# Optimization experiments

Hardware: AMD Instinct MI355X
Metric: run time of the kernel (lower is better)

Reference implementation:

```python
import jax, jax.numpy as jnp
import numpy as np

N_NODES = 100000
N_EDGES = 1600000
D_IN = 128
D_HID = 128
D_OUT = 128


def setup_inputs() -> dict:
    key = jax.random.key(0)
    ks = jax.random.split(key, 9)
    x = jax.random.normal(ks[0], (N_NODES, D_IN), dtype=jnp.float32)
    src = jax.random.randint(ks[1], (N_EDGES,), 0, N_NODES, dtype=jnp.int32)
    dst = jax.random.randint(ks[2], (N_EDGES,), 0, N_NODES, dtype=jnp.int32)
    s = 1.0 / np.sqrt(D_IN)
    Wc = jax.random.uniform(ks[3], (D_IN, D_HID), dtype=jnp.float32, minval=-s, maxval=s)
    bc = jnp.zeros((D_HID,), dtype=jnp.float32)
    s1 = 1.0 / np.sqrt(D_HID)
    W1 = jax.random.uniform(ks[4], (D_HID, D_HID), dtype=jnp.float32, minval=-s1, maxval=s1)
    b1 = jax.random.uniform(ks[5], (D_HID,), dtype=jnp.float32, minval=-s1, maxval=s1)
    W2 = jax.random.uniform(ks[6], (D_HID, D_OUT), dtype=jnp.float32, minval=-s1, maxval=s1)
    b2 = jax.random.uniform(ks[7], (D_OUT,), dtype=jnp.float32, minval=-s1, maxval=s1)
    return {"x": x, "src": src, "dst": dst, "Wc": Wc, "bc": bc,
            "W1": W1, "b1": b1, "W2": W2, "b2": b2}


def reference(x, src, dst, Wc, bc, W1, b1, W2, b2):
    # DGL GraphConv with norm='both' (default), no edge_weight:
    #   h = x / sqrt(out_deg(src));  agg[v] = sum_{(u->v)} h[u];  agg /= sqrt(in_deg(v))
    ones = jnp.ones((src.shape[0],), dtype=x.dtype)
    deg_out = jax.ops.segment_sum(ones, src, num_segments=N_NODES)
    deg_in = jax.ops.segment_sum(ones, dst, num_segments=N_NODES)
    norm_out = jax.lax.rsqrt(jnp.clip(deg_out, 1.0))[:, None]  # [N,1]
    norm_in = jax.lax.rsqrt(jnp.clip(deg_in, 1.0))[:, None]

    h = x * norm_out
    msgs = h[src]                                              # [E, D_in]
    agg = jax.ops.segment_sum(msgs, dst, num_segments=N_NODES) # [N, D_in]
    agg = agg * norm_in
    h = agg @ Wc + bc                                          # GraphConv linear

    # num_layers == 2 path: relu -> fc -> relu -> fc2
    h = jax.nn.relu(h)
    h = h @ W1 + b1
    h = jax.nn.relu(h)
    out = h @ W2 + b2
    return out
```

## Files before the change

### kernel.cpp

```cpp
#include <hip/hip_runtime.h>
#include <hip/hip_fp16.h>

#define NN 100000
#define NE 1600000
#define NBK 782
#define MAXB 2560
#define EPB 4096
#define NPB 391

typedef __attribute__((ext_vector_type(8))) __bf16 bf16x8;
typedef __attribute__((ext_vector_type(4))) float f32x4;

__global__ __launch_bounds__(256) void initcur_kernel(int* __restrict__ cursorA,
                                                      int* __restrict__ cursorO) {
    int b = blockIdx.x * 256 + threadIdx.x;
    if (b < NBK) { cursorA[b] = b * MAXB; cursorO[b] = b * MAXB; }
}

__global__ __launch_bounds__(256) void phase1_kernel(const int* __restrict__ src,
                                                     const int* __restrict__ dst,
                                                     int* __restrict__ cursorA,
                                                     int* __restrict__ cursorO,
                                                     int* __restrict__ tempA,
                                                     unsigned char* __restrict__ tempO8) {
    __shared__ int cntA[NBK], cntO[NBK];
    const int t = threadIdx.x;
    for (int b = t; b < NBK; b += 256) { cntA[b] = 0; cntO[b] = 0; }
    __syncthreads();
    const int e0 = blockIdx.x * EPB;
    int rD[16], rS[16];
#pragma unroll
    for (int i = 0; i < 16; ++i) {
        int e = e0 + i * 256 + t;
        if (e < NE) {
            rD[i] = atomicAdd(&cntA[dst[e] >> 7], 1);
            rS[i] = atomicAdd(&cntO[src[e] >> 7], 1);
        }
    }
    __syncthreads();
    for (int b = t; b < NBK; b += 256) {
        int c = cntA[b];
        cntA[b] = c ? atomicAdd(&cursorA[b], c) : 0;
        c = cntO[b];
        cntO[b] = c ? atomicAdd(&cursorO[b], c) : 0;
    }
    __syncthreads();
#pragma unroll
    for (int i = 0; i < 16; ++i) {
        int e = e0 + i * 256 + t;
        if (e < NE) {
            int d = dst[e], s = src[e];
            tempA[cntA[d >> 7] + rD[i]] = ((d & 127) << 17) | s;
            tempO8[cntO[s >> 7] + rS[i]] = (unsigned char)(s & 127);
        }
    }
}

__global__ __launch_bounds__(1024) void bscan_kernel(const int* __restrict__ cursorA,
                                                     int* __restrict__ edgeBase) {
    __shared__ int sm[1024];
    int t = threadIdx.x;
    int v = (t < NBK) ? (cursorA[t] - t * MAXB) : 0;
    sm[t] = v;
    __syncthreads();
    for (int o = 1; o < 1024; o <<= 1) {
        int u = (t >= o) ? sm[t - o] : 0;
        __syncthreads();
        sm[t] += u;
        __syncthreads();
    }
    if (t < NBK) edgeBase[t] = sm[t] - v;
}

__global__ __launch_bounds__(256) void phase2_kernel(const int* __restrict__ cursorA,
                                                     const int* __restrict__ cursorO,
                                                     const int* __restrict__ tempA,
                                                     const unsigned char* __restrict__ tempO8,
                                                     const int* __restrict__ edgeBase,
                                                     const float* __restrict__ x,
                                                     int* __restrict__ csr_src,
                                                     int* __restrict__ rowptr,
                                                     float* __restrict__ normI,
                                                     __half* __restrict__ xh) {
    __shared__ int buf[MAXB];
    __shared__ int cnt[128], ex[128], run[128], cntO[128];
    const int b = blockIdx.x;
    const int t = threadIdx.x;
    const int cA = cursorA[b] - b * MAXB;
    const int cO = cursorO[b] - b * MAXB;
    const int base = edgeBase[b];
    if (t < 128) { cnt[t] = 0; cntO[t] = 0; run[t] = 0; }
    __syncthreads();
    for (int i = t; i < cA; i += 256) {
        int w = tempA[b * MAXB + i];
        buf[i] = w;
        atomicAdd(&cnt[(w >> 17) & 127], 1);
    }
    for (int i = t; i < cO; i += 256)
        atomicAdd(&cntO[tempO8[b * MAXB + i]], 1);
    __syncthreads();
    {
        int r = t >> 1;
        int node = b * 128 + r;
        if (node < NN) {
            float nO = rsqrtf(fmaxf((float)cntO[r], 1.0f));
            int c0 = (t & 1) * 64;
#pragma unroll
            for (int i = 0; i < 16; ++i) {
                float4 v = *reinterpret_cast<const float4*>(&x[(size_t)node * 128 + c0 + i * 4]);
                __half2 h01 = __floats2half2_rn(v.x * nO, v.y * nO);
                __half2 h23 = __floats2half2_rn(v.z * nO, v.w * nO);
                __half2 hh[2] = {h01, h23};
                *reinterpret_cast<float2*>(&xh[(size_t)node * 128 + c0 + i * 4]) =
                    *reinterpret_cast<float2*>(hh);
            }
        }
    }
    if (t < 128) ex[t] = cnt[t];
    __syncthreads();
    for (int o = 1; o < 128; o <<= 1) {
        int u = (t >= o && t < 128) ? ex[t - o] : 0;
        __syncthreads();
        if (t < 128) ex[t] += u;
        __syncthreads();
    }
    if (t < 128) {
        int node = b * 128 + t;
        if (node < NN) {
            rowptr[node] = base + ex[t] - cnt[t];
            normI[node] = rsqrtf(fmaxf((float)cnt[t], 1.0f));
        }
    }
    if (b == 0 && t == 0) rowptr[NN] = NE;
    __syncthreads();
    for (int i = t; i < cA; i += 256) {
        int w = buf[i];
        int n = (w >> 17) & 127;
        int r = atomicAdd(&run[n], 1);
        csr_src[base + ex[n] - cnt[n] + r] = w & 0x1FFFF;
    }
}

__global__ __launch_bounds__(256) void gather_kernel(const __half* __restrict__ xh,
                                                     const int* __restrict__ rowptr,
                                                     const int* __restrict__ csr_src,
                                                     const float* __restrict__ normI,
                                                     float* __restrict__ agg) {
    int node = blockIdx.x * 8 + (threadIdx.x >> 5);
    int lane = threadIdx.x & 31;
    if (node >= NN) return;
    int beg = rowptr[node], end = rowptr[node + 1];
    float ax = 0.f, ay = 0.f, az = 0.f, aw = 0.f;
    int j = beg;
    for (; j + 4 <= end; j += 4) {
        int s0 = csr_src[j], s1 = csr_src[j + 1], s2 = csr_src[j + 2], s3 = csr_src[j + 3];
        float2 r0 = *reinterpret_cast<const float2*>(&xh[(size_t)s0 * 128 + lane * 4]);
        float2 r1 = *reinterpret_cast<const float2*>(&xh[(size_t)s1 * 128 + lane * 4]);
        float2 r2 = *reinterpret_cast<const float2*>(&xh[(size_t)s2 * 128 + lane * 4]);
        float2 r3 = *reinterpret_cast<const float2*>(&xh[(size_t)s3 * 128 + lane * 4]);
        const __half2* p0 = reinterpret_cast<const __half2*>(&r0);
        const __half2* p1 = reinterpret_cast<const __half2*>(&r1);
        const __half2* p2 = reinterpret_cast<const __half2*>(&r2);
        const __half2* p3 = reinterpret_cast<const __half2*>(&r3);
        float2 l0 = __half22float2(p0[0]), h0 = __half22float2(p0[1]);
        float2 l1 = __half22float2(p1[0]), h1 = __half22float2(p1[1]);
        float2 l2 = __half22float2(p2[0]), h2 = __half22float2(p2[1]);
        float2 l3 = __half22float2(p3[0]), h3 = __half22float2(p3[1]);
        ax += l0.x + l1.x + l2.x + l3.x;
        ay += l0.y + l1.y + l2.y + l3.y;
        az += h0.x + h1.x + h2.x + h3.x;
        aw += h0.y + h1.y + h2.y + h3.y;
    }
    for (; j < end; ++j) {
        int s = csr_src[j];
        float2 r = *reinterpret_cast<const float2*>(&xh[(size_t)s * 128 + lane * 4]);
        const __half2* p = reinterpret_cast<const __half2*>(&r);
        float2 l = __half22float2(p[0]), h = __half22float2(p[1]);
        ax += l.x; ay += l.y; az += h.x; aw += h.y;
    }
    float ni = normI[node];
    float4 o = make_float4(ax * ni, ay * ni, az * ni, aw * ni);
    *reinterpret_cast<float4*>(&agg[(size_t)node * 128 + lane * 4]) = o;
}

__global__ __launch_bounds__(256) void wprep_kernel(const float* __restrict__ Wc,
                                                    const float* __restrict__ W1,
                                                    const float* __restrict__ W2,
                                                    __bf16* __restrict__ Wf) {
    int t = blockIdx.x * 256 + threadIdx.x;
    if (t >= 3 * 4 * 8 * 64) return;
    int lane = t & 63;
    int ct = (t >> 6) & 7;
    int kt = (t >> 9) & 3;
    int layer = t >> 11;
    const float* W = (layer == 0) ? Wc : (layer == 1) ? W1 : W2;
    int c = ct * 16 + (lane & 15);
    int kbase = kt * 32 + (lane >> 4) * 8;
    bf16x8 hi, lo;
#pragma unroll
    for (int j = 0; j < 8; ++j) {
        float wv = W[(size_t)(kbase + j) * 128 + c];
        __bf16 h = (__bf16)wv;
        hi[j] = h;
        lo[j] = (__bf16)(wv - (float)h);
    }
    bf16x8* Wv = reinterpret_cast<bf16x8*>(Wf);
    Wv[((size_t)((layer * 2 + 0) * 4 + kt) * 8 + ct) * 64 + lane] = hi;
    Wv[((size_t)((layer * 2 + 1) * 4 + kt) * 8 + ct) * 64 + lane] = lo;
}

struct MlpState {
    f32x4 acc[8];
    bf16x8 ahi, alo;
    float bv[3][8];
};

#define ISSUE_CHUNK(GL, GKT, GH, SLOT)                                          \
    {                                                                           \
        _Pragma("unroll") for (int i = 0; i < 2; ++i) {                         \
            int s = wv * 2 + i;                                                 \
            int h = s >> 2, ctl = s & 3;                                        \
            size_t goff = ((size_t)((((GL)*2 + h) * 4 + (GKT)) * 8 + (GH)*4 + ctl)) * 1024 \
                        + (size_t)lane * 16;                                    \
            __builtin_amdgcn_global_load_lds(                                   \
                (const __attribute__((address_space(1))) unsigned int*)(Wb + goff), \
                (__attribute__((address_space(3))) unsigned int*)(&WL[SLOT][s * 1024]), \
                16, 0, 0);                                                      \
        }                                                                       \
    }

template <int C>
__device__ __forceinline__ void mstep(const char* __restrict__ Wb,
                                      char (&WL)[5][8192],
                                      float (&HS)[64][132],
                                      MlpState& st,
                                      float* __restrict__ Cout, int n, int row0,
                                      int tid, int lane, int wv, int mrow, int kg) {
    constexpr int layer = C >> 3;
    constexpr int kt = (C >> 1) & 3;
    constexpr int half = C & 1;
    constexpr int VM = (C < 20) ? 6 : 0;

    asm volatile("s_waitcnt vmcnt(%0)" ::"i"(VM) : "memory");
    __builtin_amdgcn_s_barrier();

    if constexpr (C + 4 < 24) {
        constexpr int g = C + 4;
        constexpr int gl = g >> 3, gkt = (g >> 1) & 3, gh = g & 1;
        ISSUE_CHUNK(gl, gkt, gh, g % 5)
    }

    if constexpr ((C & 7) == 0) {
#pragma unroll
        for (int i = 0; i < 8; ++i) st.acc[i] = (f32x4){0.f, 0.f, 0.f, 0.f};
    }
    if constexpr (half == 0) {
        const float* hsrc = &HS[wv * 16 + mrow][kt * 32 + kg * 8];
        float4 p0 = *reinterpret_cast<const float4*>(hsrc);
        float4 p1 = *reinterpret_cast<const float4*>(hsrc + 4);
        float av[8] = {p0.x, p0.y, p0.z, p0.w, p1.x, p1.y, p1.z, p1.w};
#pragma unroll
        for (int j = 0; j < 8; ++j) {
            __bf16 h = (__bf16)av[j];
            st.ahi[j] = h;
            st.alo[j] = (__bf16)(av[j] - (float)h);
        }
    }

    const bf16x8* WB = reinterpret_cast<const bf16x8*>(&WL[C % 5][0]);
    bf16x8 bhi[4], blo[4];
#pragma unroll
    for (int q = 0; q < 4; ++q) {
        bhi[q] = WB[q * 64 + lane];
        blo[q] = WB[(4 + q) * 64 + lane];
    }
#pragma unroll
    for (int q = 0; q < 4; ++q) {
        const int ct = half * 4 + q;
        st.acc[ct] = __builtin_amdgcn_mfma_f32_16x16x32_bf16(st.alo, bhi[q], st.acc[ct], 0, 0, 0);
        st.acc[ct] = __builtin_amdgcn_mfma_f32_16x16x32_bf16(st.ahi, blo[q], st.acc[ct], 0, 0, 0);
        st.acc[ct] = __builtin_amdgcn_mfma_f32_16x16x32_bf16(st.ahi, bhi[q], st.acc[ct], 0, 0, 0);
    }

    if constexpr ((C & 7) == 7) {
        if constexpr (layer < 2) {
#pragma unroll
            for (int ct = 0; ct < 8; ++ct)
#pragma unroll
                for (int r = 0; r < 4; ++r)
                    HS[wv * 16 + kg * 4 + r][ct * 16 + mrow] =
                        fmaxf(st.acc[ct][r] + st.bv[layer][ct], 0.f);
            asm volatile("s_waitcnt lgkmcnt(0)" ::: "memory");
        } else {
#pragma unroll
            for (int ct = 0; ct < 8; ++ct)
#pragma unroll
                for (int r = 0; r < 4; ++r) {
                    int grow = row0 + wv * 16 + kg * 4 + r;
                    if (grow < n)
                        Cout[(size_t)grow * 128 + ct * 16 + mrow] = st.acc[ct][r] + st.bv[2][ct];
                }
        }
    }
}

__global__ __launch_bounds__(256, 2) void mlp_mfma(const float* __restrict__ A,
                                                   const __bf16* __restrict__ Wf,
                                                   const float* __restrict__ bc,
                                                   const float* __restrict__ b1,
                                                   const float* __restrict__ b2,
                                                   float* __restrict__ C, int n) {
    __shared__ float HS[64][132];
    __shared__ char WL[5][8192];
    const int tid = threadIdx.x;
    const int lane = tid & 63;
    const int wv = tid >> 6;
    const int row0 = blockIdx.x * 64;
    const int mrow = lane & 15;
    const int kg = lane >> 4;
    const char* Wb = (const char*)Wf;

    ISSUE_CHUNK(0, 0, 0, 0)
    ISSUE_CHUNK(0, 0, 1, 1)
    ISSUE_CHUNK(0, 1, 0, 2)
    ISSUE_CHUNK(0, 1, 1, 3)

    {
        int r = tid >> 5;
        int c4 = (tid & 31) * 4;
#pragma unroll
        for (int i = 0; i < 8; ++i) {
            int row = i * 8 + r;
            int grow = row0 + row;
            float4 v = make_float4(0.f, 0.f, 0.f, 0.f);
            if (grow < n)
                v = *reinterpret_cast<const float4*>(&A[(size_t)grow * 128 + c4]);
            *reinterpret_cast<float4*>(&HS[row][c4]) = v;
        }
    }
    MlpState st;
#pragma unroll
    for (int ct = 0; ct < 8; ++ct) {
        st.bv[0][ct] = bc[ct * 16 + mrow];
        st.bv[1][ct] = b1[ct * 16 + mrow];
        st.bv[2][ct] = b2[ct * 16 + mrow];
    }
    __syncthreads();

    mstep<0>(Wb, WL, HS, st, C, n, row0, tid, lane, wv, mrow, kg);
    mstep<1>(Wb, WL, HS, st, C, n, row0, tid, lane, wv, mrow, kg);
    mstep<2>(Wb, WL, HS, st, C, n, row0, tid, lane, wv, mrow, kg);
    mstep<3>(Wb, WL, HS, st, C, n, row0, tid, lane, wv, mrow, kg);
    mstep<4>(Wb, WL, HS, st, C, n, row0, tid, lane, wv, mrow, kg);
    mstep<5>(Wb, WL, HS, st, C, n, row0, tid, lane, wv, mrow, kg);
    mstep<6>(Wb, WL, HS, st, C, n, row0, tid, lane, wv, mrow, kg);
    mstep<7>(Wb, WL, HS, st, C, n, row0, tid, lane, wv, mrow, kg);
    mstep<8>(Wb, WL, HS, st, C, n, row0, tid, lane, wv, mrow, kg);
    mstep<9>(Wb, WL, HS, st, C, n, row0, tid, lane, wv, mrow, kg);
    mstep<10>(Wb, WL, HS, st, C, n, row0, tid, lane, wv, mrow, kg);
    mstep<11>(Wb, WL, HS, st, C, n, row0, tid, lane, wv, mrow, kg);
    mstep<12>(Wb, WL, HS, st, C, n, row0, tid, lane, wv, mrow, kg);
    mstep<13>(Wb, WL, HS, st, C, n, row0, tid, lane, wv, mrow, kg);
    mstep<14>(Wb, WL, HS, st, C, n, row0, tid, lane, wv, mrow, kg);
    mstep<15>(Wb, WL, HS, st, C, n, row0, tid, lane, wv, mrow, kg);
    mstep<16>(Wb, WL, HS, st, C, n, row0, tid, lane, wv, mrow, kg);
    mstep<17>(Wb, WL, HS, st, C, n, row0, tid, lane, wv, mrow, kg);
    mstep<18>(Wb, WL, HS, st, C, n, row0, tid, lane, wv, mrow, kg);
    mstep<19>(Wb, WL, HS, st, C, n, row0, tid, lane, wv, mrow, kg);
    mstep<20>(Wb, WL, HS, st, C, n, row0, tid, lane, wv, mrow, kg);
    mstep<21>(Wb, WL, HS, st, C, n, row0, tid, lane, wv, mrow, kg);
    mstep<22>(Wb, WL, HS, st, C, n, row0, tid, lane, wv, mrow, kg);
    mstep<23>(Wb, WL, HS, st, C, n, row0, tid, lane, wv, mrow, kg);
}

extern "C" void kernel_launch(void* const* d_in, const int* in_sizes, int n_in,
                              void* d_out, int out_size, void* d_ws, size_t ws_size,
                              hipStream_t stream) {
    const float* x  = (const float*)d_in[0];
    const int*  src = (const int*)d_in[1];
    const int*  dst = (const int*)d_in[2];
    const float* Wc = (const float*)d_in[3];
    const float* bc = (const float*)d_in[4];
    const float* W1 = (const float*)d_in[5];
    const float* b1 = (const float*)d_in[6];
    const float* W2 = (const float*)d_in[7];
    const float* b2 = (const float*)d_in[8];
    float* out = (float*)d_out;

    char* p = (char*)d_ws;
    __bf16* Wf = (__bf16*)p;            p += 196608;
    __half* xh = (__half*)p;            p += (size_t)NN * 128 * 2;
    int* tempA = (int*)p;               p += (size_t)NBK * MAXB * 4;
    unsigned char* tempO8 = (unsigned char*)p; p += (size_t)NBK * MAXB;
    int* cursorA  = (int*)p;            p += (size_t)NBK * 4;
    int* cursorO  = (int*)p;            p += (size_t)NBK * 4;
    int* edgeBase = (int*)p;            p += (size_t)NBK * 4;
    int* rowptr   = (int*)p;            p += (size_t)(NN + 1) * 4;
    float* normI  = (float*)p;          p += (size_t)NN * 4;
    int* csr_src  = (int*)p;

    wprep_kernel<<<24, 256, 0, stream>>>(Wc, W1, W2, Wf);
    initcur_kernel<<<(NBK + 255) / 256, 256, 0, stream>>>(cursorA, cursorO);
    phase1_kernel<<<NPB, 256, 0, stream>>>(src, dst, cursorA, cursorO, tempA, tempO8);
    bscan_kernel<<<1, 1024, 0, stream>>>(cursorA, edgeBase);
    phase2_kernel<<<NBK, 256, 0, stream>>>(cursorA, cursorO, tempA, tempO8, edgeBase,
                                           x, csr_src, rowptr, normI, xh);

    gather_kernel<<<(NN + 7) / 8, 256, 0, stream>>>(xh, rowptr, csr_src, normI, out);

    mlp_mfma<<<(NN + 63) / 64, 256, 0, stream>>>(out, Wf, bc, b1, b2, out, NN);
}
```

Measured before the change: 213.1 us.

## Fuse neighbor gather aggregation into MLP kernel via shared memory

Removes the separate gather kernel and performs the CSR neighbor sum for each 64-row tile directly inside the MLP kernel, writing the normalized aggregate into the shared HS buffer instead of global memory. This drops a 51 MB fp32 write and re-read of the aggregate plus one kernel launch. The in-degree norm is now recomputed from rowptr rather than read from normI. In exchange, the latency-bound gather now runs inside a kernel with heavy LDS use and limited occupancy (launch bounds of 2), so it may hide memory latency less well than the standalone gather did.

New measurement: 282.1 us. +32.3%, slower.

```diff
diff --git a/kernel.cpp b/kernel.cpp
--- a/kernel.cpp
+++ b/kernel.cpp
@@ -141,48 +141,6 @@
     }
 }
 
-__global__ __launch_bounds__(256) void gather_kernel(const __half* __restrict__ xh,
-                                                     const int* __restrict__ rowptr,
-                                                     const int* __restrict__ csr_src,
-                                                     const float* __restrict__ normI,
-                                                     float* __restrict__ agg) {
-    int node = blockIdx.x * 8 + (threadIdx.x >> 5);
-    int lane = threadIdx.x & 31;
-    if (node >= NN) return;
-    int beg = rowptr[node], end = rowptr[node + 1];
-    float ax = 0.f, ay = 0.f, az = 0.f, aw = 0.f;
-    int j = beg;
-    for (; j + 4 <= end; j += 4) {
-        int s0 = csr_src[j], s1 = csr_src[j + 1], s2 = csr_src[j + 2], s3 = csr_src[j + 3];
-        float2 r0 = *reinterpret_cast<const float2*>(&xh[(size_t)s0 * 128 + lane * 4]);
-        float2 r1 = *reinterpret_cast<const float2*>(&xh[(size_t)s1 * 128 + lane * 4]);
-        float2 r2 = *reinterpret_cast<const float2*>(&xh[(size_t)s2 * 128 + lane * 4]);
-        float2 r3 = *reinterpret_cast<const float2*>(&xh[(size_t)s3 * 128 + lane * 4]);
-        const __half2* p0 = reinterpret_cast<const __half2*>(&r0);
-        const __half2* p1 = reinterpret_cast<const __half2*>(&r1);
-        const __half2* p2 = reinterpret_cast<const __half2*>(&r2);
-        const __half2* p3 = reinterpret_cast<const __half2*>(&r3);
-        float2 l0 = __half22float2(p0[0]), h0 = __half22float2(p0[1]);
-        float2 l1 = __half22float2(p1[0]), h1 = __half22float2(p1[1]);
-        float2 l2 = __half22float2(p2[0]), h2 = __half22float2(p2[1]);
-        float2 l3 = __half22float2(p3[0]), h3 = __half22float2(p3[1]);
-        ax += l0.x + l1.x + l2.x + l3.x;
-        ay += l0.y + l1.y + l2.y + l3.y;
-        az += h0.x + h1.x + h2.x + h3.x;
-        aw += h0.y + h1.y + h2.y + h3.y;
-    }
-    for (; j < end; ++j) {
-        int s = csr_src[j];
-        float2 r = *reinterpret_cast<const float2*>(&xh[(size_t)s * 128 + lane * 4]);
-        const __half2* p = reinterpret_cast<const __half2*>(&r);
-        float2 l = __half22float2(p[0]), h = __half22float2(p[1]);
-        ax += l.x; ay += l.y; az += h.x; aw += h.y;
-    }
-    float ni = normI[node];
-    float4 o = make_float4(ax * ni, ay * ni, az * ni, aw * ni);
-    *reinterpret_cast<float4*>(&agg[(size_t)node * 128 + lane * 4]) = o;
-}
-
 __global__ __launch_bounds__(256) void wprep_kernel(const float* __restrict__ Wc,
                                                     const float* __restrict__ W1,
                                                     const float* __restrict__ W2,
@@ -235,7 +193,7 @@
                                       float (&HS)[64][132],
                                       MlpState& st,
                                       float* __restrict__ Cout, int n, int row0,
-                                      int tid, int lane, int wv, int mrow, int kg) {
+                                      int lane, int wv, int mrow, int kg) {
     constexpr int layer = C >> 3;
     constexpr int kt = (C >> 1) & 3;
     constexpr int half = C & 1;
@@ -304,12 +262,14 @@
     }
 }
 
-__global__ __launch_bounds__(256, 2) void mlp_mfma(const float* __restrict__ A,
-                                                   const __bf16* __restrict__ Wf,
-                                                   const float* __restrict__ bc,
-                                                   const float* __restrict__ b1,
-                                                   const float* __restrict__ b2,
-                                                   float* __restrict__ C, int n) {
+__global__ __launch_bounds__(256, 2) void fused_gmlp(const __half* __restrict__ xh,
+                                                     const int* __restrict__ rowptr,
+                                                     const int* __restrict__ csr_src,
+                                                     const __bf16* __restrict__ Wf,
+                                                     const float* __restrict__ bc,
+                                                     const float* __restrict__ b1,
+                                                     const float* __restrict__ b2,
+                                                     float* __restrict__ C, int n) {
     __shared__ float HS[64][132];
     __shared__ char WL[5][8192];
     const int tid = threadIdx.x;
@@ -326,18 +286,51 @@
     ISSUE_CHUNK(0, 1, 1, 3)
 
     {
-        int r = tid >> 5;
-        int c4 = (tid & 31) * 4;
-#pragma unroll
-        for (int i = 0; i < 8; ++i) {
-            int row = i * 8 + r;
-            int grow = row0 + row;
-            float4 v = make_float4(0.f, 0.f, 0.f, 0.f);
-            if (grow < n)
-                v = *reinterpret_cast<const float4*>(&A[(size_t)grow * 128 + c4]);
-            *reinterpret_cast<float4*>(&HS[row][c4]) = v;
-        }
-    }
+        const int w32 = tid >> 5;
+        const int l32 = tid & 31;
+#pragma unroll
+        for (int it = 0; it < 8; ++it) {
+            int nl = it * 8 + w32;
+            int node = row0 + nl;
+            float ax = 0.f, ay = 0.f, az = 0.f, aw = 0.f;
+            float ni = 0.f;
+            if (node < NN) {
+                int beg = rowptr[node], end = rowptr[node + 1];
+                ni = rsqrtf(fmaxf((float)(end - beg), 1.0f));
+                int j = beg;
+                for (; j + 4 <= end; j += 4) {
+                    int s0 = csr_src[j], s1 = csr_src[j + 1];
+                    int s2 = csr_src[j + 2], s3 = csr_src[j + 3];
+                    float2 r0 = *reinterpret_cast<const float2*>(&xh[(size_t)s0 * 128 + l32 * 4]);
+                    float2 r1 = *reinterpret_cast<const float2*>(&xh[(size_t)s1 * 128 + l32 * 4]);
+                    float2 r2 = *reinterpret_cast<const float2*>(&xh[(size_t)s2 * 128 + l32 * 4]);
+                    float2 r3 = *reinterpret_cast<const float2*>(&xh[(size_t)s3 * 128 + l32 * 4]);
+                    const __half2* p0 = reinterpret_cast<const __half2*>(&r0);
+                    const __half2* p1 = reinterpret_cast<const __half2*>(&r1);
+                    const __half2* p2 = reinterpret_cast<const __half2*>(&r2);
+                    const __half2* p3 = reinterpret_cast<const __half2*>(&r3);
+                    float2 l0 = __half22float2(p0[0]), h0 = __half22float2(p0[1]);
+                    float2 l1 = __half22float2(p1[0]), h1 = __half22float2(p1[1]);
+                    float2 l2 = __half22float2(p2[0]), h2 = __half22float2(p2[1]);
+                    float2 l3 = __half22float2(p3[0]), h3 = __half22float2(p3[1]);
+                    ax += l0.x + l1.x + l2.x + l3.x;
+                    ay += l0.y + l1.y + l2.y + l3.y;
+                    az += h0.x + h1.x + h2.x + h3.x;
+                    aw += h0.y + h1.y + h2.y + h3.y;
+                }
+                for (; j < end; ++j) {
+                    int s = csr_src[j];
+                    float2 r = *reinterpret_cast<const float2*>(&xh[(size_t)s * 128 + l32 * 4]);
+                    const __half2* p = reinterpret_cast<const __half2*>(&r);
+                    float2 l = __half22float2(p[0]), h = __half22float2(p[1]);
+                    ax += l.x; ay += l.y; az += h.x; aw += h.y;
+                }
+            }
+            *reinterpret_cast<float4*>(&HS[nl][l32 * 4]) =
+                make_float4(ax * ni, ay * ni, az * ni, aw * ni);
+        }
+    }
+
     MlpState st;
 #pragma unroll
     for (int ct = 0; ct < 8; ++ct) {
@@ -347,30 +340,30 @@
     }
     __syncthreads();
 
-    mstep<0>(Wb, WL, HS, st, C, n, row0, tid, lane, wv, mrow, kg);
-    mstep<1>(Wb, WL, HS, st, C, n, row0, tid, lane, wv, mrow, kg);
-    mstep<2>(Wb, WL, HS, st, C, n, row0, tid, lane, wv, mrow, kg);
-    mstep<3>(Wb, WL, HS, st, C, n, row0, tid, lane, wv, mrow, kg);
-    mstep<4>(Wb, WL, HS, st, C, n, row0, tid, lane, wv, mrow, kg);
-    mstep<5>(Wb, WL, HS, st, C, n, row0, tid, lane, wv, mrow, kg);
-    mstep<6>(Wb, WL, HS, st, C, n, row0, tid, lane, wv, mrow, kg);
-    mstep<7>(Wb, WL, HS, st, C, n, row0, tid, lane, wv, mrow, kg);
-    mstep<8>(Wb, WL, HS, st, C, n, row0, tid, lane, wv, mrow, kg);
-    mstep<9>(Wb, WL, HS, st, C, n, row0, tid, lane, wv, mrow, kg);
-    mstep<10>(Wb, WL, HS, st, C, n, row0, tid, lane, wv, mrow, kg);
-    mstep<11>(Wb, WL, HS, st, C, n, row0, tid, lane, wv, mrow, kg);
-    mstep<12>(Wb, WL, HS, st, C, n, row0, tid, lane, wv, mrow, kg);
-    mstep<13>(Wb, WL, HS, st, C, n, row0, tid, lane, wv, mrow, kg);
-    mstep<14>(Wb, WL, HS, st, C, n, row0, tid, lane, wv, mrow, kg);
-    mstep<15>(Wb, WL, HS, st, C, n, row0, tid, lane, wv, mrow, kg);
-    mstep<16>(Wb, WL, HS, st, C, n, row0, tid, lane, wv, mrow, kg);
-    mstep<17>(Wb, WL, HS, st, C, n, row0, tid, lane, wv, mrow, kg);
-    mstep<18>(Wb, WL, HS, st, C, n, row0, tid, lane, wv, mrow, kg);
-    mstep<19>(Wb, WL, HS, st, C, n, row0, tid, lane, wv, mrow, kg);
-    mstep<20>(Wb, WL, HS, st, C, n, row0, tid, lane, wv, mrow, kg);
-    mstep<21>(Wb, WL, HS, st, C, n, row0, tid, lane, wv, mrow, kg);
-    mstep<22>(Wb, WL, HS, st, C, n, row0, tid, lane, wv, mrow, kg);
-    mstep<23>(Wb, WL, HS, st, C, n, row0, tid, lane, wv, mrow, kg);
+    mstep<0>(Wb, WL, HS, st, C, n, row0, lane, wv, mrow, kg);
+    mstep<1>(Wb, WL, HS, st, C, n, row0, lane, wv, mrow, kg);
+    mstep<2>(Wb, WL, HS, st, C, n, row0, lane, wv, mrow, kg);
+    mstep<3>(Wb, WL, HS, st, C, n, row0, lane, wv, mrow, kg);
+    mstep<4>(Wb, WL, HS, st, C, n, row0, lane, wv, mrow, kg);
+    mstep<5>(Wb, WL, HS, st, C, n, row0, lane, wv, mrow, kg);
+    mstep<6>(Wb, WL, HS, st, C, n, row0, lane, wv, mrow, kg);
+    mstep<7>(Wb, WL, HS, st, C, n, row0, lane, wv, mrow, kg);
+    mstep<8>(Wb, WL, HS, st, C, n, row0, lane, wv, mrow, kg);
+    mstep<9>(Wb, WL, HS, st, C, n, row0, lane, wv, mrow, kg);
+    mstep<10>(Wb, WL, HS, st, C, n, row0, lane, wv, mrow, kg);
+    mstep<11>(Wb, WL, HS, st, C, n, row0, lane, wv, mrow, kg);
+    mstep<12>(Wb, WL, HS, st, C, n, row0, lane, wv, mrow, kg);
+    mstep<13>(Wb, WL, HS, st, C, n, row0, lane, wv, mrow, kg);
+    mstep<14>(Wb, WL, HS, st, C, n, row0, lane, wv, mrow, kg);
+    mstep<15>(Wb, WL, HS, st, C, n, row0, lane, wv, mrow, kg);
+    mstep<16>(Wb, WL, HS, st, C, n, row0, lane, wv, mrow, kg);
+    mstep<17>(Wb, WL, HS, st, C, n, row0, lane, wv, mrow, kg);
+    mstep<18>(Wb, WL, HS, st, C, n, row0, lane, wv, mrow, kg);
+    mstep<19>(Wb, WL, HS, st, C, n, row0, lane, wv, mrow, kg);
+    mstep<20>(Wb, WL, HS, st, C, n, row0, lane, wv, mrow, kg);
+    mstep<21>(Wb, WL, HS, st, C, n, row0, lane, wv, mrow, kg);
+    mstep<22>(Wb, WL, HS, st, C, n, row0, lane, wv, mrow, kg);
+    mstep<23>(Wb, WL, HS, st, C, n, row0, lane, wv, mrow, kg);
 }
 
 extern "C" void kernel_launch(void* const* d_in, const int* in_sizes, int n_in,
@@ -406,7 +399,6 @@
     phase2_kernel<<<NBK, 256, 0, stream>>>(cursorA, cursorO, tempA, tempO8, edgeBase,
                                            x, csr_src, rowptr, normI, xh);
 
-    gather_kernel<<<(NN + 7) / 8, 256, 0, stream>>>(xh, rowptr, csr_src, normI, out);
-
-    mlp_mfma<<<(NN + 63) / 64, 256, 0, stream>>>(out, Wf, bc, b1, b2, out, NN);
-}
+    fused_gmlp<<<(NN + 63) / 64, 256, 0, stream>>>(xh, rowptr, csr_src,
+                                                   Wf, bc, b1, b2, out, NN);
+}
```
